# Optimization experiments

Measured on AMD Instinct MI355X. Metric: run time of the kernel, lower is better.

Reference implementation:

```python
import jax, jax.numpy as jnp
import numpy as np

L = 2          # num_layers
H = 1024       # hidden_size
XD = 192       # exogenous feature dim
YD = 64        # out_size == y dim
IN = XD + YD   # lstm input size
B = 256
PRE_LEN = 64
FWD_LEN = 48


def setup_inputs() -> dict:
    key = jax.random.key(0)
    ks = jax.random.split(key, 16)
    s = 0.05  # keep gate pre-activations in a sane range
    inp = {
        "pre_x": jax.random.normal(ks[0], (PRE_LEN, B, XD), jnp.float32),
        "pre_y": jax.random.normal(ks[1], (PRE_LEN, B, YD), jnp.float32),
        "forward_x": jax.random.normal(ks[2], (FWD_LEN, B, XD), jnp.float32),
        # layer 0 LSTM params (torch layout: w_ih (4H, IN), w_hh (4H, H))
        "w_ih_0": jax.random.normal(ks[3], (4 * H, IN), jnp.float32) * s,
        "w_hh_0": jax.random.normal(ks[4], (4 * H, H), jnp.float32) * s,
        "b_ih_0": jax.random.normal(ks[5], (4 * H,), jnp.float32) * s,
        "b_hh_0": jax.random.normal(ks[6], (4 * H,), jnp.float32) * s,
        # layer 1
        "w_ih_1": jax.random.normal(ks[7], (4 * H, H), jnp.float32) * s,
        "w_hh_1": jax.random.normal(ks[8], (4 * H, H), jnp.float32) * s,
        "b_ih_1": jax.random.normal(ks[9], (4 * H,), jnp.float32) * s,
        "b_hh_1": jax.random.normal(ks[10], (4 * H,), jnp.float32) * s,
        # fc: Linear(H,H) -> Tanh -> Linear(H,YD)
        "fc_w1": jax.random.normal(ks[11], (H, H), jnp.float32) * s,
        "fc_b1": jax.random.normal(ks[12], (H,), jnp.float32) * s,
        "fc_w2": jax.random.normal(ks[13], (YD, H), jnp.float32) * s,
        "fc_b2": jax.random.normal(ks[14], (YD,), jnp.float32) * s,
    }
    return inp


def _lstm_cell(x, h, c, w_ih, w_hh, b_ih, b_hh):
    # torch gate order: i, f, g, o
    z = x @ w_ih.T + h @ w_hh.T + (b_ih + b_hh)  # (B, 4H)
    i, f, g, o = jnp.split(z, 4, axis=-1)
    c_new = jax.nn.sigmoid(f) * c + jax.nn.sigmoid(i) * jnp.tanh(g)
    h_new = jax.nn.sigmoid(o) * jnp.tanh(c_new)
    return h_new, c_new


def _stack_step(layers, x_t, hs, cs):
    # layers: list of (w_ih, w_hh, b_ih, b_hh); hs, cs: (L, B, H)
    new_h, new_c = [], []
    inp = x_t
    for l, (w_ih, w_hh, b_ih, b_hh) in enumerate(layers):
        h, c = _lstm_cell(inp, hs[l], cs[l], w_ih, w_hh, b_ih, b_hh)
        new_h.append(h)
        new_c.append(c)
        inp = h
    return jnp.stack(new_h), jnp.stack(new_c), inp  # inp = top-layer output


def reference(pre_x, pre_y, forward_x,
              w_ih_0, w_hh_0, b_ih_0, b_hh_0,
              w_ih_1, w_hh_1, b_ih_1, b_hh_1,
              fc_w1, fc_b1, fc_w2, fc_b2):
    layers = [(w_ih_0, w_hh_0, b_ih_0, b_hh_0),
              (w_ih_1, w_hh_1, b_ih_1, b_hh_1)]

    def fc(x):
        return jnp.tanh(x @ fc_w1.T + fc_b1) @ fc_w2.T + fc_b2

    batch = pre_x.shape[1]
    hs0 = jnp.zeros((L, batch, H), pre_x.dtype)
    cs0 = jnp.zeros((L, batch, H), pre_x.dtype)

    # --- warmup encode over concat(pre_x, pre_y) ---
    xy = jnp.concatenate([pre_x, pre_y], axis=2)  # (PRE_LEN, B, IN)

    def enc_step(carry, x_t):
        hs, cs = carry
        hs, cs, top = _stack_step(layers, x_t, hs, cs)
        return (hs, cs), top

    (hs, cs), enc_outs = jax.lax.scan(enc_step, (hs0, cs0), xy)
    top = enc_outs[-1]          # output[-1] from the encoding pass
    last_y = pre_y[-1]

    def dec_step(carry, fx_t):
        hs, cs, top, last_y = carry
        est = fc(top) + last_y                        # (B, YD)
        x_in = jnp.concatenate([fx_t, est], axis=1)   # (B, IN)
        hs, cs, top = _stack_step(layers, x_in, hs, cs)
        return (hs, cs, top, est), est

    _, est_all = jax.lax.scan(dec_step, (hs, cs, top, last_y), forward_x)
    return est_all  # (FWD_LEN, B, YD)
```

## Files before the change

### kernel.cpp

```cpp
#include <hip/hip_runtime.h>
#include <stdint.h>

typedef unsigned short u16;
typedef __attribute__((ext_vector_type(8))) _Float16 f16x8;
typedef __attribute__((ext_vector_type(4))) float f32x4;

__device__ inline f16x8 ldfrag(const u16* p) { return *(const f16x8*)p; }
__device__ inline u16 f2h(float x) {
    _Float16 h = (_Float16)x;
    union { _Float16 h; u16 u; } v; v.h = h;
    return v.u;
}
__device__ inline float sigmoidf_(float x) { return 1.0f / (1.0f + expf(-x)); }


__global__ __launch_bounds__(512, 2) void lstm_cell_k(
    const u16* __restrict__ AFa, int KBa,
    const u16* __restrict__ BFa,
    const u16* __restrict__ AFh,
    const u16* __restrict__ BFh,
    const float* __restrict__ bsum,
    float* __restrict__ c,
    u16* __restrict__ h_out)
{
    const int tid  = threadIdx.x;
    const int w    = tid >> 6;
    const int lane = tid & 63;
    const int l15  = lane & 15;
    const int quad = lane >> 4;
    const int ct   = blockIdx.x;
    const int mg   = blockIdx.y;

    f32x4 acc[4][4];
    #pragma unroll
    for (int t = 0; t < 4; ++t)
        #pragma unroll
        for (int g = 0; g < 4; ++g) acc[t][g] = (f32x4){0, 0, 0, 0};

    {
        const int q = KBa >> 3;
        #pragma unroll 2
        for (int kb = w * q; kb < w * q + q; ++kb) {
            f16x8 a[4], b[4];
            #pragma unroll
            for (int t = 0; t < 4; ++t)
                a[t] = ldfrag(AFa + (((size_t)(mg * 4 + t) * KBa + kb) * 64 + lane) * 8);
            #pragma unroll
            for (int g = 0; g < 4; ++g)
                b[g] = ldfrag(BFa + (((size_t)(ct * 4 + g) * KBa + kb) * 64 + lane) * 8);
            #pragma unroll
            for (int t = 0; t < 4; ++t)
                #pragma unroll
                for (int g = 0; g < 4; ++g)
                    acc[t][g] = __builtin_amdgcn_mfma_f32_16x16x32_f16(a[t], b[g], acc[t][g], 0, 0, 0);
        }
    }
    {
        #pragma unroll 2
        for (int kb = w * 4; kb < w * 4 + 4; ++kb) {
            f16x8 a[4], b[4];
            #pragma unroll
            for (int t = 0; t < 4; ++t)
                a[t] = ldfrag(AFh + (((size_t)(mg * 4 + t) * 32 + kb) * 64 + lane) * 8);
            #pragma unroll
            for (int g = 0; g < 4; ++g)
                b[g] = ldfrag(BFh + (((size_t)(ct * 4 + g) * 32 + kb) * 64 + lane) * 8);
            #pragma unroll
            for (int t = 0; t < 4; ++t)
                #pragma unroll
                for (int g = 0; g < 4; ++g)
                    acc[t][g] = __builtin_amdgcn_mfma_f32_16x16x32_f16(a[t], b[g], acc[t][g], 0, 0, 0);
        }
    }

    __shared__ f32x4 red[4][16][64];
    if (w >= 4) {
        #pragma unroll
        for (int t = 0; t < 4; ++t)
            #pragma unroll
            for (int g = 0; g < 4; ++g)
                red[w - 4][t * 4 + g][lane] = acc[t][g];
    }
    __syncthreads();
    if (w < 4) {
        #pragma unroll
        for (int t = 0; t < 4; ++t)
            #pragma unroll
            for (int g = 0; g < 4; ++g)
                red[w][t * 4 + g][lane] += acc[t][g];
    }
    __syncthreads();
    if (w < 4) {
        f32x4 z[4];
        #pragma unroll
        for (int g = 0; g < 4; ++g)
            z[g] = red[0][w * 4 + g][lane] + red[1][w * 4 + g][lane] +
                   red[2][w * 4 + g][lane] + red[3][w * 4 + g][lane];

        const int col   = ct * 16 + l15;
        const int mtile = mg * 4 + w;
        float bv[4];
        #pragma unroll
        for (int g = 0; g < 4; ++g) bv[g] = bsum[g * 1024 + col];
        const int hkb = col >> 5, hquad = (col >> 3) & 3, hj = col & 7;
        #pragma unroll
        for (int r = 0; r < 4; ++r) {
            const int rl  = quad * 4 + r;
            const int row = mtile * 16 + rl;
            const size_t gi = (size_t)row * 1024 + col;
            const float zi = z[0][r] + bv[0];
            const float zf = z[1][r] + bv[1];
            const float zg = z[2][r] + bv[2];
            const float zo = z[3][r] + bv[3];
            const float cv = c[gi];
            const float cn = sigmoidf_(zf) * cv + sigmoidf_(zi) * tanhf(zg);
            c[gi] = cn;
            h_out[(((size_t)mtile * 32 + hkb) * 64 + hquad * 16 + rl) * 8 + hj] =
                f2h(sigmoidf_(zo) * tanhf(cn));
        }
    }
}

__global__ __launch_bounds__(512, 2) void fc1_k(
    const u16* __restrict__ AFx,
    const u16* __restrict__ BFw,
    const float* __restrict__ bias,
    u16* __restrict__ U)
{
    const int tid  = threadIdx.x;
    const int w    = tid >> 6;
    const int lane = tid & 63;
    const int l15  = lane & 15;
    const int quad = lane >> 4;
    const int ctq  = blockIdx.x;
    const int mg   = blockIdx.y;

    f32x4 acc[4][4];
    #pragma unroll
    for (int t = 0; t < 4; ++t)
        #pragma unroll
        for (int g = 0; g < 4; ++g) acc[t][g] = (f32x4){0, 0, 0, 0};

    #pragma unroll 2
    for (int kb = w * 4; kb < w * 4 + 4; ++kb) {
        f16x8 a[4], b[4];
        #pragma unroll
        for (int t = 0; t < 4; ++t)
            a[t] = ldfrag(AFx + (((size_t)(mg * 4 + t) * 32 + kb) * 64 + lane) * 8);
        #pragma unroll
        for (int g = 0; g < 4; ++g)
            b[g] = ldfrag(BFw + (((size_t)(ctq * 4 + g) * 32 + kb) * 64 + lane) * 8);
        #pragma unroll
        for (int t = 0; t < 4; ++t)
            #pragma unroll
            for (int g = 0; g < 4; ++g)
                acc[t][g] = __builtin_amdgcn_mfma_f32_16x16x32_f16(a[t], b[g], acc[t][g], 0, 0, 0);
    }

    __shared__ f32x4 red[4][16][64];
    if (w >= 4) {
        #pragma unroll
        for (int t = 0; t < 4; ++t)
            #pragma unroll
            for (int g = 0; g < 4; ++g)
                red[w - 4][t * 4 + g][lane] = acc[t][g];
    }
    __syncthreads();
    if (w < 4) {
        #pragma unroll
        for (int t = 0; t < 4; ++t)
            #pragma unroll
            for (int g = 0; g < 4; ++g)
                red[w][t * 4 + g][lane] += acc[t][g];
    }
    __syncthreads();
    if (w < 4) {
        f32x4 z[4];
        #pragma unroll
        for (int g = 0; g < 4; ++g)
            z[g] = red[0][w * 4 + g][lane] + red[1][w * 4 + g][lane] +
                   red[2][w * 4 + g][lane] + red[3][w * 4 + g][lane];

        const int mtile = mg * 4 + w;
        #pragma unroll
        for (int g = 0; g < 4; ++g) {
            const int col = ctq * 64 + g * 16 + l15;
            const float bv = bias[col];
            const int ukb = col >> 5, uquad = (col >> 3) & 3, uj = col & 7;
            #pragma unroll
            for (int r = 0; r < 4; ++r) {
                const int rl = quad * 4 + r;
                U[(((size_t)mtile * 32 + ukb) * 64 + uquad * 16 + rl) * 8 + uj] =
                    f2h(tanhf(z[g][r] + bv));
            }
        }
    }
}

__global__ __launch_bounds__(512) void fc2_k(
    const u16* __restrict__ AFu,
    const u16* __restrict__ BFw2,
    const float* __restrict__ b2,
    float* __restrict__ est_prev,
    float* __restrict__ out_t,
    u16* __restrict__ xdec_t)
{
    const int tid  = threadIdx.x;
    const int w    = tid >> 6;
    const int lane = tid & 63;
    const int l15  = lane & 15;
    const int quad = lane >> 4;
    const int mtile = blockIdx.x;
    const int cg = w & 3;
    const int kh = w >> 2;

    f32x4 accp[4] = {{0,0,0,0},{0,0,0,0},{0,0,0,0},{0,0,0,0}};
    const u16* ap = AFu + ((size_t)(mtile * 32 + kh * 16) * 64 + lane) * 8;
    const u16* bp = BFw2 + ((size_t)(cg * 32 + kh * 16) * 64 + lane) * 8;
    #pragma unroll 4
    for (int kb = 0; kb < 16; ++kb)
        accp[kb & 3] = __builtin_amdgcn_mfma_f32_16x16x32_f16(
            ldfrag(ap + kb * 512), ldfrag(bp + kb * 512), accp[kb & 3], 0, 0, 0);
    f32x4 acc = accp[0] + accp[1] + accp[2] + accp[3];

    __shared__ f32x4 r2[8][64];
    r2[w][lane] = acc;
    __syncthreads();
    if (w < 4) {
        acc = r2[w][lane] + r2[w + 4][lane];

        const int col = w * 16 + l15;
        const float bv = b2[col];
        const int cx = 192 + col;
        const int xkb = cx >> 5, xquad = (cx >> 3) & 3, xj = cx & 7;
        #pragma unroll
        for (int r = 0; r < 4; ++r) {
            const int rl = quad * 4 + r;
            const int row = mtile * 16 + rl;
            const float v = acc[r] + bv + est_prev[row * 64 + col];
            est_prev[row * 64 + col] = v;
            out_t[row * 64 + col] = v;
            xdec_t[(((size_t)mtile * 8 + xkb) * 64 + xquad * 16 + rl) * 8 + xj] = f2h(v);
        }
    }
}

__global__ void cvt_bfrag_k(const float* __restrict__ src, u16* __restrict__ dst,
                            int K, int kbshift, int S1, int S2, int total) {
    int i = blockIdx.x * 256 + threadIdx.x;
    if (i >= total) return;
    const int lane = i & 63;
    const int kb   = (i >> 6) & ((1 << kbshift) - 1);
    const int rest = i >> (6 + kbshift);
    const int sub  = rest & 3;
    const int grp  = rest >> 2;
    const int row  = sub * S1 + grp * S2 + (lane & 15);
    const int colK = kb * 32 + (lane >> 4) * 8;
    const float* s = src + (size_t)row * K + colK;
    u16* d = dst + (size_t)i * 8;
    #pragma unroll
    for (int j = 0; j < 8; ++j) d[j] = f2h(s[j]);
}
__global__ void bias_k(const float* __restrict__ a, const float* __restrict__ b,
                       float* __restrict__ d, int n) {
    int i = blockIdx.x * 256 + threadIdx.x;
    if (i < n) d[i] = a[i] + b[i];
}
__global__ void init_k(u16* h0, u16* h1, float* c0, float* c1) {
    int i = blockIdx.x * 256 + threadIdx.x;
    h0[i] = 0; h1[i] = 0; c0[i] = 0.0f; c1[i] = 0.0f;
}
__global__ void estinit_k(const float* __restrict__ pre_y, float* __restrict__ est_prev) {
    int i = blockIdx.x * 256 + threadIdx.x;
    est_prev[i] = pre_y[63 * 16384 + i];
}
__global__ void pack_enc_k(const float* __restrict__ pre_x, const float* __restrict__ pre_y,
                           u16* __restrict__ xy) {
    int i = blockIdx.x * 256 + threadIdx.x;
    const int lane  = i & 63;
    const int kb    = (i >> 6) & 7;
    const int mtile = (i >> 9) & 15;
    const int t     = i >> 13;
    const int row   = mtile * 16 + (lane & 15);
    const int cb    = kb * 32 + (lane >> 4) * 8;
    u16* d = xy + (size_t)i * 8;
    #pragma unroll
    for (int j = 0; j < 8; ++j) {
        const int col = cb + j;
        const float v = (col < 192) ? pre_x[((size_t)t * 256 + row) * 192 + col]
                                    : pre_y[((size_t)t * 256 + row) * 64 + (col - 192)];
        d[j] = f2h(v);
    }
}
__global__ void pack_dec_k(const float* __restrict__ fx, u16* __restrict__ xd,
                           int total_threads) {
    int i = blockIdx.x * 256 + threadIdx.x;
    if (i >= total_threads) return;
    const int lane  = i & 63;
    int rest = i >> 6;
    const int kb    = rest % 6;  rest /= 6;
    const int mtile = rest & 15;
    const int t     = rest >> 4;
    const int row   = mtile * 16 + (lane & 15);
    const int cb    = kb * 32 + (lane >> 4) * 8;
    u16* d = xd + ((((size_t)t * 16 + mtile) * 8 + kb) * 64 + lane) * 8;
    #pragma unroll
    for (int j = 0; j < 8; ++j)
        d[j] = f2h(fx[((size_t)t * 256 + row) * 192 + cb + j]);
}

extern "C" void kernel_launch(void* const* d_in, const int* in_sizes, int n_in,
                              void* d_out, int out_size, void* d_ws, size_t ws_size,
                              hipStream_t stream) {
    const float* pre_x  = (const float*)d_in[0];
    const float* pre_y  = (const float*)d_in[1];
    const float* fx     = (const float*)d_in[2];
    const float* w_ih_0 = (const float*)d_in[3];
    const float* w_hh_0 = (const float*)d_in[4];
    const float* b_ih_0 = (const float*)d_in[5];
    const float* b_hh_0 = (const float*)d_in[6];
    const float* w_ih_1 = (const float*)d_in[7];
    const float* w_hh_1 = (const float*)d_in[8];
    const float* b_ih_1 = (const float*)d_in[9];
    const float* b_hh_1 = (const float*)d_in[10];
    const float* fc_w1  = (const float*)d_in[11];
    const float* fc_b1  = (const float*)d_in[12];
    const float* fc_w2  = (const float*)d_in[13];
    const float* fc_b2  = (const float*)d_in[14];

    size_t off = 0;
    char* wsb = (char*)d_ws;
    auto alloc = [&](size_t bytes) -> void* {
        void* p = wsb + off;
        off += (bytes + 255) & ~(size_t)255;
        return p;
    };
    u16* wih0 = (u16*)alloc((size_t)4096 * 256 * 2);
    u16* whh0 = (u16*)alloc((size_t)4096 * 1024 * 2);
    u16* wih1 = (u16*)alloc((size_t)4096 * 1024 * 2);
    u16* whh1 = (u16*)alloc((size_t)4096 * 1024 * 2);
    u16* fcw1 = (u16*)alloc((size_t)1024 * 1024 * 2);
    u16* fcw2 = (u16*)alloc((size_t)64 * 1024 * 2);
    float* b0s = (float*)alloc(4096 * 4);
    float* b1s = (float*)alloc(4096 * 4);
    u16* xyenc = (u16*)alloc((size_t)64 * 256 * 256 * 2);
    u16* xdec  = (u16*)alloc((size_t)48 * 256 * 256 * 2);
    u16* h0b[2] = { (u16*)alloc((size_t)256 * 1024 * 2), (u16*)alloc((size_t)256 * 1024 * 2) };
    u16* h1b[2] = { (u16*)alloc((size_t)256 * 1024 * 2), (u16*)alloc((size_t)256 * 1024 * 2) };
    float* c0 = (float*)alloc((size_t)256 * 1024 * 4);
    float* c1 = (float*)alloc((size_t)256 * 1024 * 4);
    u16* ufc  = (u16*)alloc((size_t)256 * 1024 * 2);
    float* estp = (float*)alloc((size_t)256 * 64 * 4);

    cvt_bfrag_k<<<512, 256, 0, stream>>>(w_ih_0, wih0, 256, 3, 1024, 16, 64 * 4 * 8 * 64);
    cvt_bfrag_k<<<2048, 256, 0, stream>>>(w_hh_0, whh0, 1024, 5, 1024, 16, 64 * 4 * 32 * 64);
    cvt_bfrag_k<<<2048, 256, 0, stream>>>(w_ih_1, wih1, 1024, 5, 1024, 16, 64 * 4 * 32 * 64);
    cvt_bfrag_k<<<2048, 256, 0, stream>>>(w_hh_1, whh1, 1024, 5, 1024, 16, 64 * 4 * 32 * 64);
    cvt_bfrag_k<<<512, 256, 0, stream>>>(fc_w1, fcw1, 1024, 5, 16, 64, 16 * 4 * 32 * 64);
    cvt_bfrag_k<<<32, 256, 0, stream>>>(fc_w2, fcw2, 1024, 5, 16, 0, 1 * 4 * 32 * 64);
    bias_k<<<16, 256, 0, stream>>>(b_ih_0, b_hh_0, b0s, 4096);
    bias_k<<<16, 256, 0, stream>>>(b_ih_1, b_hh_1, b1s, 4096);
    init_k<<<1024, 256, 0, stream>>>(h0b[0], h1b[0], c0, c1);
    estinit_k<<<64, 256, 0, stream>>>(pre_y, estp);
    pack_enc_k<<<2048, 256, 0, stream>>>(pre_x, pre_y, xyenc);
    pack_dec_k<<<1152, 256, 0, stream>>>(fx, xdec, 48 * 16 * 6 * 64);

    int cur = 0;
    for (int t = 0; t < 64; ++t) {
        lstm_cell_k<<<dim3(64, 4), 512, 0, stream>>>(
            xyenc + (size_t)t * 65536, 8, wih0, h0b[cur], whh0, b0s, c0, h0b[1 - cur]);
        lstm_cell_k<<<dim3(64, 4), 512, 0, stream>>>(
            h0b[1 - cur], 32, wih1, h1b[cur], whh1, b1s, c1, h1b[1 - cur]);
        cur ^= 1;
    }
    float* out = (float*)d_out;
    for (int t = 0; t < 48; ++t) {
        fc1_k<<<dim3(16, 4), 512, 0, stream>>>(h1b[cur], fcw1, fc_b1, ufc);
        fc2_k<<<16, 512, 0, stream>>>(ufc, fcw2, fc_b2, estp,
                                      out + (size_t)t * 16384,
                                      xdec + (size_t)t * 65536);
        lstm_cell_k<<<dim3(64, 4), 512, 0, stream>>>(
            xdec + (size_t)t * 65536, 8, wih0, h0b[cur], whh0, b0s, c0, h0b[1 - cur]);
        lstm_cell_k<<<dim3(64, 4), 512, 0, stream>>>(
            h0b[1 - cur], 32, wih1, h1b[cur], whh1, b1s, c1, h1b[1 - cur]);
        cur ^= 1;
    }
}
```

Before: 3.858 ms.

## Replace per-step kernel launches with a persistent cooperative kernel using grid sync

The many per-timestep launches (two LSTM cells per step, plus fc1/fc2 in decode) become one cooperative persistent kernel of 256 blocks that steps through all timesteps, separated by grid-wide barriers. Cell state and the running estimate stay in registers instead of global memory. fc1 and fc2 are re-tiled to match the fixed 256-block grid. The aim is to remove launch overhead and c-state traffic, at the cost of grid.sync latency and needing all 256 blocks to be co-resident. The last decode step's LSTM update is skipped because its output is never used.

```diff
diff --git a/kernel.cpp b/kernel.cpp
--- a/kernel.cpp
+++ b/kernel.cpp
@@ -1,5 +1,8 @@
 #include <hip/hip_runtime.h>
+#include <hip/hip_cooperative_groups.h>
 #include <stdint.h>
+
+namespace cg = cooperative_groups;
 
 typedef unsigned short u16;
 typedef __attribute__((ext_vector_type(8))) _Float16 f16x8;
@@ -14,233 +17,253 @@
 __device__ inline float sigmoidf_(float x) { return 1.0f / (1.0f + expf(-x)); }
 
 
-__global__ __launch_bounds__(512, 2) void lstm_cell_k(
-    const u16* __restrict__ AFa, int KBa,
-    const u16* __restrict__ BFa,
-    const u16* __restrict__ AFh,
-    const u16* __restrict__ BFh,
-    const float* __restrict__ bsum,
-    float* __restrict__ c,
-    u16* __restrict__ h_out)
+struct PP {
+    const u16* xyenc;
+    u16* xdec;
+    const u16 *wih0, *whh0, *wih1, *whh1, *fcw1, *fcw2;
+    const float *b0s, *b1s, *fcb1, *fcb2, *pre_y;
+    u16 *h0a, *h0b, *h1a, *h1b, *ufc;
+    float* out;
+};
+
+static __device__ __forceinline__ void lstm_phase(
+    const u16* __restrict__ AFa, int KBa, const u16* __restrict__ BFa,
+    const u16* __restrict__ AFh, const u16* __restrict__ BFh,
+    const float* __restrict__ bsum, float* creg, u16* __restrict__ h_out,
+    int ct, int mg, int w, int lane, f32x4 (*red)[16][64])
 {
+    const int l15  = lane & 15;
+    const int quad = lane >> 4;
+
+    f32x4 acc[4][4];
+    #pragma unroll
+    for (int t = 0; t < 4; ++t)
+        #pragma unroll
+        for (int g = 0; g < 4; ++g) acc[t][g] = (f32x4){0, 0, 0, 0};
+
+    {
+        const int q = KBa >> 3;
+        #pragma unroll 2
+        for (int kb = w * q; kb < w * q + q; ++kb) {
+            f16x8 a[4], b[4];
+            #pragma unroll
+            for (int t = 0; t < 4; ++t)
+                a[t] = ldfrag(AFa + (((size_t)(mg * 4 + t) * KBa + kb) * 64 + lane) * 8);
+            #pragma unroll
+            for (int g = 0; g < 4; ++g)
+                b[g] = ldfrag(BFa + (((size_t)(ct * 4 + g) * KBa + kb) * 64 + lane) * 8);
+            #pragma unroll
+            for (int t = 0; t < 4; ++t)
+                #pragma unroll
+                for (int g = 0; g < 4; ++g)
+                    acc[t][g] = __builtin_amdgcn_mfma_f32_16x16x32_f16(a[t], b[g], acc[t][g], 0, 0, 0);
+        }
+    }
+    {
+        #pragma unroll 2
+        for (int kb = w * 4; kb < w * 4 + 4; ++kb) {
+            f16x8 a[4], b[4];
+            #pragma unroll
+            for (int t = 0; t < 4; ++t)
+                a[t] = ldfrag(AFh + (((size_t)(mg * 4 + t) * 32 + kb) * 64 + lane) * 8);
+            #pragma unroll
+            for (int g = 0; g < 4; ++g)
+                b[g] = ldfrag(BFh + (((size_t)(ct * 4 + g) * 32 + kb) * 64 + lane) * 8);
+            #pragma unroll
+            for (int t = 0; t < 4; ++t)
+                #pragma unroll
+                for (int g = 0; g < 4; ++g)
+                    acc[t][g] = __builtin_amdgcn_mfma_f32_16x16x32_f16(a[t], b[g], acc[t][g], 0, 0, 0);
+        }
+    }
+
+    if (w >= 4) {
+        #pragma unroll
+        for (int t = 0; t < 4; ++t)
+            #pragma unroll
+            for (int g = 0; g < 4; ++g)
+                red[w - 4][t * 4 + g][lane] = acc[t][g];
+    }
+    __syncthreads();
+    if (w < 4) {
+        #pragma unroll
+        for (int t = 0; t < 4; ++t)
+            #pragma unroll
+            for (int g = 0; g < 4; ++g)
+                red[w][t * 4 + g][lane] += acc[t][g];
+    }
+    __syncthreads();
+    if (w < 4) {
+        f32x4 z[4];
+        #pragma unroll
+        for (int g = 0; g < 4; ++g)
+            z[g] = red[0][w * 4 + g][lane] + red[1][w * 4 + g][lane] +
+                   red[2][w * 4 + g][lane] + red[3][w * 4 + g][lane];
+
+        const int col   = ct * 16 + l15;
+        const int mtile = mg * 4 + w;
+        float bv[4];
+        #pragma unroll
+        for (int g = 0; g < 4; ++g) bv[g] = bsum[g * 1024 + col];
+        const int hkb = col >> 5, hquad = (col >> 3) & 3, hj = col & 7;
+        #pragma unroll
+        for (int r = 0; r < 4; ++r) {
+            const int rl = quad * 4 + r;
+            const float zi = z[0][r] + bv[0];
+            const float zf = z[1][r] + bv[1];
+            const float zg = z[2][r] + bv[2];
+            const float zo = z[3][r] + bv[3];
+            const float cv = creg[r];
+            const float cn = sigmoidf_(zf) * cv + sigmoidf_(zi) * tanhf(zg);
+            creg[r] = cn;
+            h_out[(((size_t)mtile * 32 + hkb) * 64 + hquad * 16 + rl) * 8 + hj] =
+                f2h(sigmoidf_(zo) * tanhf(cn));
+        }
+    }
+}
+
+static __device__ __forceinline__ void fc1_phase(
+    const u16* __restrict__ AFx, const u16* __restrict__ BFw,
+    const float* __restrict__ bias, u16* __restrict__ U,
+    int b, int w, int lane, f32x4 (*red)[16][64])
+{
+    const int mt = b >> 4, ctq = b & 15;
+    const int l15 = lane & 15, quad = lane >> 4;
+    f32x4 acc[4];
+    #pragma unroll
+    for (int g = 0; g < 4; ++g) acc[g] = (f32x4){0, 0, 0, 0};
+
+    #pragma unroll
+    for (int k = 0; k < 4; ++k) {
+        const int kb = w * 4 + k;
+        f16x8 a = ldfrag(AFx + (((size_t)mt * 32 + kb) * 64 + lane) * 8);
+        #pragma unroll
+        for (int g = 0; g < 4; ++g) {
+            f16x8 bb = ldfrag(BFw + (((size_t)(ctq * 4 + g) * 32 + kb) * 64 + lane) * 8);
+            acc[g] = __builtin_amdgcn_mfma_f32_16x16x32_f16(a, bb, acc[g], 0, 0, 0);
+        }
+    }
+
+    f32x4 (*r8)[4][64] = (f32x4 (*)[4][64])red;
+    #pragma unroll
+    for (int g = 0; g < 4; ++g) r8[w][g][lane] = acc[g];
+    __syncthreads();
+    if (w < 4) {
+        f32x4 z = r8[0][w][lane];
+        #pragma unroll
+        for (int p = 1; p < 8; ++p) z += r8[p][w][lane];
+        const int col = ctq * 64 + w * 16 + l15;
+        const float bv = bias[col];
+        const int ukb = col >> 5, uq = (col >> 3) & 3, uj = col & 7;
+        #pragma unroll
+        for (int r = 0; r < 4; ++r) {
+            const int rl = quad * 4 + r;
+            U[(((size_t)mt * 32 + ukb) * 64 + uq * 16 + rl) * 8 + uj] =
+                f2h(tanhf(z[r] + bv));
+        }
+    }
+}
+
+static __device__ __forceinline__ void fc2_phase(
+    const u16* __restrict__ AFu, const u16* __restrict__ BFw2,
+    const float* __restrict__ b2, float* estreg,
+    float* __restrict__ out_t, u16* __restrict__ xdec_t,
+    int b, int w, int lane, f32x4 (*red)[16][64])
+{
+    f32x4 (*rr)[64] = (f32x4 (*)[64])red;
+    const int l15 = lane & 15, quad = lane >> 4;
+    const int mt = b >> 2, cg = b & 3;
+    if (b < 64) {
+        f32x4 acc = (f32x4){0, 0, 0, 0};
+        #pragma unroll
+        for (int k = 0; k < 4; ++k) {
+            const int kb = w * 4 + k;
+            acc = __builtin_amdgcn_mfma_f32_16x16x32_f16(
+                ldfrag(AFu + (((size_t)mt * 32 + kb) * 64 + lane) * 8),
+                ldfrag(BFw2 + (((size_t)cg * 32 + kb) * 64 + lane) * 8), acc, 0, 0, 0);
+        }
+        rr[w][lane] = acc;
+    }
+    __syncthreads();
+    if (b < 64 && w == 0) {
+        f32x4 acc = rr[0][lane];
+        #pragma unroll
+        for (int p = 1; p < 8; ++p) acc += rr[p][lane];
+        const int col = cg * 16 + l15;
+        const float bv = b2[col];
+        const int cx = 192 + col;
+        const int xkb = cx >> 5, xq = (cx >> 3) & 3, xj = cx & 7;
+        #pragma unroll
+        for (int r = 0; r < 4; ++r) {
+            const int rl = quad * 4 + r;
+            const int row = mt * 16 + rl;
+            const float v = acc[r] + bv + estreg[r];
+            estreg[r] = v;
+            out_t[row * 64 + col] = v;
+            xdec_t[(((size_t)mt * 8 + xkb) * 64 + xq * 16 + rl) * 8 + xj] = f2h(v);
+        }
+    }
+}
+
+__global__ __launch_bounds__(512, 2) void persist_k(PP p)
+{
+    cg::grid_group grid = cg::this_grid();
+    __shared__ f32x4 red[4][16][64];
+
     const int tid  = threadIdx.x;
     const int w    = tid >> 6;
     const int lane = tid & 63;
     const int l15  = lane & 15;
     const int quad = lane >> 4;
-    const int ct   = blockIdx.x;
-    const int mg   = blockIdx.y;
-
-    f32x4 acc[4][4];
-    #pragma unroll
-    for (int t = 0; t < 4; ++t)
-        #pragma unroll
-        for (int g = 0; g < 4; ++g) acc[t][g] = (f32x4){0, 0, 0, 0};
-
-    {
-        const int q = KBa >> 3;
-        #pragma unroll 2
-        for (int kb = w * q; kb < w * q + q; ++kb) {
-            f16x8 a[4], b[4];
-            #pragma unroll
-            for (int t = 0; t < 4; ++t)
-                a[t] = ldfrag(AFa + (((size_t)(mg * 4 + t) * KBa + kb) * 64 + lane) * 8);
-            #pragma unroll
-            for (int g = 0; g < 4; ++g)
-                b[g] = ldfrag(BFa + (((size_t)(ct * 4 + g) * KBa + kb) * 64 + lane) * 8);
-            #pragma unroll
-            for (int t = 0; t < 4; ++t)
-                #pragma unroll
-                for (int g = 0; g < 4; ++g)
-                    acc[t][g] = __builtin_amdgcn_mfma_f32_16x16x32_f16(a[t], b[g], acc[t][g], 0, 0, 0);
-        }
-    }
-    {
-        #pragma unroll 2
-        for (int kb = w * 4; kb < w * 4 + 4; ++kb) {
-            f16x8 a[4], b[4];
-            #pragma unroll
-            for (int t = 0; t < 4; ++t)
-                a[t] = ldfrag(AFh + (((size_t)(mg * 4 + t) * 32 + kb) * 64 + lane) * 8);
-            #pragma unroll
-            for (int g = 0; g < 4; ++g)
-                b[g] = ldfrag(BFh + (((size_t)(ct * 4 + g) * 32 + kb) * 64 + lane) * 8);
-            #pragma unroll
-            for (int t = 0; t < 4; ++t)
-                #pragma unroll
-                for (int g = 0; g < 4; ++g)
-                    acc[t][g] = __builtin_amdgcn_mfma_f32_16x16x32_f16(a[t], b[g], acc[t][g], 0, 0, 0);
-        }
-    }
-
-    __shared__ f32x4 red[4][16][64];
-    if (w >= 4) {
-        #pragma unroll
-        for (int t = 0; t < 4; ++t)
-            #pragma unroll
-            for (int g = 0; g < 4; ++g)
-                red[w - 4][t * 4 + g][lane] = acc[t][g];
-    }
-    __syncthreads();
-    if (w < 4) {
-        #pragma unroll
-        for (int t = 0; t < 4; ++t)
-            #pragma unroll
-            for (int g = 0; g < 4; ++g)
-                red[w][t * 4 + g][lane] += acc[t][g];
-    }
-    __syncthreads();
-    if (w < 4) {
-        f32x4 z[4];
-        #pragma unroll
-        for (int g = 0; g < 4; ++g)
-            z[g] = red[0][w * 4 + g][lane] + red[1][w * 4 + g][lane] +
-                   red[2][w * 4 + g][lane] + red[3][w * 4 + g][lane];
-
-        const int col   = ct * 16 + l15;
-        const int mtile = mg * 4 + w;
-        float bv[4];
-        #pragma unroll
-        for (int g = 0; g < 4; ++g) bv[g] = bsum[g * 1024 + col];
-        const int hkb = col >> 5, hquad = (col >> 3) & 3, hj = col & 7;
+    const int b    = blockIdx.x;
+    const int ct   = b & 63;
+    const int mg   = b >> 6;
+
+    float c0reg[4] = {0.f, 0.f, 0.f, 0.f};
+    float c1reg[4] = {0.f, 0.f, 0.f, 0.f};
+    float estreg[4] = {0.f, 0.f, 0.f, 0.f};
+    if (b < 64) {
+        const int fmt = b >> 2, fcg = b & 3;
         #pragma unroll
         for (int r = 0; r < 4; ++r) {
-            const int rl  = quad * 4 + r;
-            const int row = mtile * 16 + rl;
-            const size_t gi = (size_t)row * 1024 + col;
-            const float zi = z[0][r] + bv[0];
-            const float zf = z[1][r] + bv[1];
-            const float zg = z[2][r] + bv[2];
-            const float zo = z[3][r] + bv[3];
-            const float cv = c[gi];
-            const float cn = sigmoidf_(zf) * cv + sigmoidf_(zi) * tanhf(zg);
-            c[gi] = cn;
-            h_out[(((size_t)mtile * 32 + hkb) * 64 + hquad * 16 + rl) * 8 + hj] =
-                f2h(sigmoidf_(zo) * tanhf(cn));
-        }
-    }
-}
-
-__global__ __launch_bounds__(512, 2) void fc1_k(
-    const u16* __restrict__ AFx,
-    const u16* __restrict__ BFw,
-    const float* __restrict__ bias,
-    u16* __restrict__ U)
-{
-    const int tid  = threadIdx.x;
-    const int w    = tid >> 6;
-    const int lane = tid & 63;
-    const int l15  = lane & 15;
-    const int quad = lane >> 4;
-    const int ctq  = blockIdx.x;
-    const int mg   = blockIdx.y;
-
-    f32x4 acc[4][4];
-    #pragma unroll
-    for (int t = 0; t < 4; ++t)
-        #pragma unroll
-        for (int g = 0; g < 4; ++g) acc[t][g] = (f32x4){0, 0, 0, 0};
-
-    #pragma unroll 2
-    for (int kb = w * 4; kb < w * 4 + 4; ++kb) {
-        f16x8 a[4], b[4];
-        #pragma unroll
-        for (int t = 0; t < 4; ++t)
-            a[t] = ldfrag(AFx + (((size_t)(mg * 4 + t) * 32 + kb) * 64 + lane) * 8);
-        #pragma unroll
-        for (int g = 0; g < 4; ++g)
-            b[g] = ldfrag(BFw + (((size_t)(ctq * 4 + g) * 32 + kb) * 64 + lane) * 8);
-        #pragma unroll
-        for (int t = 0; t < 4; ++t)
-            #pragma unroll
-            for (int g = 0; g < 4; ++g)
-                acc[t][g] = __builtin_amdgcn_mfma_f32_16x16x32_f16(a[t], b[g], acc[t][g], 0, 0, 0);
-    }
-
-    __shared__ f32x4 red[4][16][64];
-    if (w >= 4) {
-        #pragma unroll
-        for (int t = 0; t < 4; ++t)
-            #pragma unroll
-            for (int g = 0; g < 4; ++g)
-                red[w - 4][t * 4 + g][lane] = acc[t][g];
-    }
-    __syncthreads();
-    if (w < 4) {
-        #pragma unroll
-        for (int t = 0; t < 4; ++t)
-            #pragma unroll
-            for (int g = 0; g < 4; ++g)
-                red[w][t * 4 + g][lane] += acc[t][g];
-    }
-    __syncthreads();
-    if (w < 4) {
-        f32x4 z[4];
-        #pragma unroll
-        for (int g = 0; g < 4; ++g)
-            z[g] = red[0][w * 4 + g][lane] + red[1][w * 4 + g][lane] +
-                   red[2][w * 4 + g][lane] + red[3][w * 4 + g][lane];
-
-        const int mtile = mg * 4 + w;
-        #pragma unroll
-        for (int g = 0; g < 4; ++g) {
-            const int col = ctq * 64 + g * 16 + l15;
-            const float bv = bias[col];
-            const int ukb = col >> 5, uquad = (col >> 3) & 3, uj = col & 7;
-            #pragma unroll
-            for (int r = 0; r < 4; ++r) {
-                const int rl = quad * 4 + r;
-                U[(((size_t)mtile * 32 + ukb) * 64 + uquad * 16 + rl) * 8 + uj] =
-                    f2h(tanhf(z[g][r] + bv));
-            }
-        }
-    }
-}
-
-__global__ __launch_bounds__(512) void fc2_k(
-    const u16* __restrict__ AFu,
-    const u16* __restrict__ BFw2,
-    const float* __restrict__ b2,
-    float* __restrict__ est_prev,
-    float* __restrict__ out_t,
-    u16* __restrict__ xdec_t)
-{
-    const int tid  = threadIdx.x;
-    const int w    = tid >> 6;
-    const int lane = tid & 63;
-    const int l15  = lane & 15;
-    const int quad = lane >> 4;
-    const int mtile = blockIdx.x;
-    const int cg = w & 3;
-    const int kh = w >> 2;
-
-    f32x4 accp[4] = {{0,0,0,0},{0,0,0,0},{0,0,0,0},{0,0,0,0}};
-    const u16* ap = AFu + ((size_t)(mtile * 32 + kh * 16) * 64 + lane) * 8;
-    const u16* bp = BFw2 + ((size_t)(cg * 32 + kh * 16) * 64 + lane) * 8;
-    #pragma unroll 4
-    for (int kb = 0; kb < 16; ++kb)
-        accp[kb & 3] = __builtin_amdgcn_mfma_f32_16x16x32_f16(
-            ldfrag(ap + kb * 512), ldfrag(bp + kb * 512), accp[kb & 3], 0, 0, 0);
-    f32x4 acc = accp[0] + accp[1] + accp[2] + accp[3];
-
-    __shared__ f32x4 r2[8][64];
-    r2[w][lane] = acc;
-    __syncthreads();
-    if (w < 4) {
-        acc = r2[w][lane] + r2[w + 4][lane];
-
-        const int col = w * 16 + l15;
-        const float bv = b2[col];
-        const int cx = 192 + col;
-        const int xkb = cx >> 5, xquad = (cx >> 3) & 3, xj = cx & 7;
-        #pragma unroll
-        for (int r = 0; r < 4; ++r) {
-            const int rl = quad * 4 + r;
-            const int row = mtile * 16 + rl;
-            const float v = acc[r] + bv + est_prev[row * 64 + col];
-            est_prev[row * 64 + col] = v;
-            out_t[row * 64 + col] = v;
-            xdec_t[(((size_t)mtile * 8 + xkb) * 64 + xquad * 16 + rl) * 8 + xj] = f2h(v);
+            const int row = fmt * 16 + quad * 4 + r;
+            const int col = fcg * 16 + l15;
+            estreg[r] = p.pre_y[(size_t)63 * 16384 + row * 64 + col];
+        }
+    }
+
+    u16 *h0c = p.h0a, *h0n = p.h0b;
+    u16 *h1c = p.h1a, *h1n = p.h1b;
+
+    for (int t = 0; t < 64; ++t) {
+        lstm_phase(p.xyenc + (size_t)t * 65536, 8, p.wih0, h0c, p.whh0,
+                   p.b0s, c0reg, h0n, ct, mg, w, lane, red);
+        grid.sync();
+        lstm_phase(h0n, 32, p.wih1, h1c, p.whh1,
+                   p.b1s, c1reg, h1n, ct, mg, w, lane, red);
+        grid.sync();
+        u16* tmp;
+        tmp = h0c; h0c = h0n; h0n = tmp;
+        tmp = h1c; h1c = h1n; h1n = tmp;
+    }
+
+    for (int t = 0; t < 48; ++t) {
+        fc1_phase(h1c, p.fcw1, p.fcb1, p.ufc, b, w, lane, red);
+        grid.sync();
+        fc2_phase(p.ufc, p.fcw2, p.fcb2, estreg,
+                  p.out + (size_t)t * 16384, p.xdec + (size_t)t * 65536,
+                  b, w, lane, red);
+        grid.sync();
+        if (t < 47) {
+            lstm_phase(p.xdec + (size_t)t * 65536, 8, p.wih0, h0c, p.whh0,
+                       p.b0s, c0reg, h0n, ct, mg, w, lane, red);
+            grid.sync();
+            lstm_phase(h0n, 32, p.wih1, h1c, p.whh1,
+                       p.b1s, c1reg, h1n, ct, mg, w, lane, red);
+            grid.sync();
+            u16* tmp;
+            tmp = h0c; h0c = h0n; h0n = tmp;
+            tmp = h1c; h1c = h1n; h1n = tmp;
         }
     }
 }
@@ -266,13 +289,9 @@
     int i = blockIdx.x * 256 + threadIdx.x;
     if (i < n) d[i] = a[i] + b[i];
 }
-__global__ void init_k(u16* h0, u16* h1, float* c0, float* c1) {
-    int i = blockIdx.x * 256 + threadIdx.x;
-    h0[i] = 0; h1[i] = 0; c0[i] = 0.0f; c1[i] = 0.0f;
-}
-__global__ void estinit_k(const float* __restrict__ pre_y, float* __restrict__ est_prev) {
-    int i = blockIdx.x * 256 + threadIdx.x;
-    est_prev[i] = pre_y[63 * 16384 + i];
+__global__ void zeroh_k(u16* h0, u16* h1) {
+    int i = blockIdx.x * 256 + threadIdx.x;
+    h0[i] = 0; h1[i] = 0;
 }
 __global__ void pack_enc_k(const float* __restrict__ pre_x, const float* __restrict__ pre_y,
                            u16* __restrict__ xy) {
@@ -345,12 +364,11 @@
     float* b1s = (float*)alloc(4096 * 4);
     u16* xyenc = (u16*)alloc((size_t)64 * 256 * 256 * 2);
     u16* xdec  = (u16*)alloc((size_t)48 * 256 * 256 * 2);
-    u16* h0b[2] = { (u16*)alloc((size_t)256 * 1024 * 2), (u16*)alloc((size_t)256 * 1024 * 2) };
-    u16* h1b[2] = { (u16*)alloc((size_t)256 * 1024 * 2), (u16*)alloc((size_t)256 * 1024 * 2) };
-    float* c0 = (float*)alloc((size_t)256 * 1024 * 4);
-    float* c1 = (float*)alloc((size_t)256 * 1024 * 4);
-    u16* ufc  = (u16*)alloc((size_t)256 * 1024 * 2);
-    float* estp = (float*)alloc((size_t)256 * 64 * 4);
+    u16* h0a = (u16*)alloc((size_t)256 * 1024 * 2);
+    u16* h0b = (u16*)alloc((size_t)256 * 1024 * 2);
+    u16* h1a = (u16*)alloc((size_t)256 * 1024 * 2);
+    u16* h1b = (u16*)alloc((size_t)256 * 1024 * 2);
+    u16* ufc = (u16*)alloc((size_t)256 * 1024 * 2);
 
     cvt_bfrag_k<<<512, 256, 0, stream>>>(w_ih_0, wih0, 256, 3, 1024, 16, 64 * 4 * 8 * 64);
     cvt_bfrag_k<<<2048, 256, 0, stream>>>(w_hh_0, whh0, 1024, 5, 1024, 16, 64 * 4 * 32 * 64);
@@ -360,29 +378,19 @@
     cvt_bfrag_k<<<32, 256, 0, stream>>>(fc_w2, fcw2, 1024, 5, 16, 0, 1 * 4 * 32 * 64);
     bias_k<<<16, 256, 0, stream>>>(b_ih_0, b_hh_0, b0s, 4096);
     bias_k<<<16, 256, 0, stream>>>(b_ih_1, b_hh_1, b1s, 4096);
-    init_k<<<1024, 256, 0, stream>>>(h0b[0], h1b[0], c0, c1);
-    estinit_k<<<64, 256, 0, stream>>>(pre_y, estp);
+    zeroh_k<<<1024, 256, 0, stream>>>(h0a, h1a);
     pack_enc_k<<<2048, 256, 0, stream>>>(pre_x, pre_y, xyenc);
     pack_dec_k<<<1152, 256, 0, stream>>>(fx, xdec, 48 * 16 * 6 * 64);
 
-    int cur = 0;
-    for (int t = 0; t < 64; ++t) {
-        lstm_cell_k<<<dim3(64, 4), 512, 0, stream>>>(
-            xyenc + (size_t)t * 65536, 8, wih0, h0b[cur], whh0, b0s, c0, h0b[1 - cur]);
-        lstm_cell_k<<<dim3(64, 4), 512, 0, stream>>>(
-            h0b[1 - cur], 32, wih1, h1b[cur], whh1, b1s, c1, h1b[1 - cur]);
-        cur ^= 1;
-    }
-    float* out = (float*)d_out;
-    for (int t = 0; t < 48; ++t) {
-        fc1_k<<<dim3(16, 4), 512, 0, stream>>>(h1b[cur], fcw1, fc_b1, ufc);
-        fc2_k<<<16, 512, 0, stream>>>(ufc, fcw2, fc_b2, estp,
-                                      out + (size_t)t * 16384,
-                                      xdec + (size_t)t * 65536);
-        lstm_cell_k<<<dim3(64, 4), 512, 0, stream>>>(
-            xdec + (size_t)t * 65536, 8, wih0, h0b[cur], whh0, b0s, c0, h0b[1 - cur]);
-        lstm_cell_k<<<dim3(64, 4), 512, 0, stream>>>(
-            h0b[1 - cur], 32, wih1, h1b[cur], whh1, b1s, c1, h1b[1 - cur]);
-        cur ^= 1;
-    }
-}
+    PP p;
+    p.xyenc = xyenc; p.xdec = xdec;
+    p.wih0 = wih0; p.whh0 = whh0; p.wih1 = wih1; p.whh1 = whh1;
+    p.fcw1 = fcw1; p.fcw2 = fcw2;
+    p.b0s = b0s; p.b1s = b1s; p.fcb1 = fc_b1; p.fcb2 = fc_b2; p.pre_y = pre_y;
+    p.h0a = h0a; p.h0b = h0b; p.h1a = h1a; p.h1b = h1b; p.ufc = ufc;
+    p.out = (float*)d_out;
+
+    void* args[] = { &p };
+    hipLaunchCooperativeKernel((const void*)persist_k, dim3(256), dim3(512),
+                               args, 0, stream);
+}
```

New measurement: 11.97 ms. 3.1x slower.
